# Kernel optimization log

Hardware: AMD Instinct MI355X
Metric: run time of the kernel (lower is better)

## Reference

```python
import jax, jax.numpy as jnp
import numpy as np

EMBED = 1024
HEADS = 16
HEAD_DIM = EMBED // HEADS


def setup_inputs() -> dict:
    key = jax.random.key(0)
    ks = jax.random.split(key, 11)
    B, L, D = 2, 2048, EMBED
    s = 0.02
    return {
        "q": jax.random.normal(ks[0], (B, L, D), jnp.float32),
        "k": jax.random.normal(ks[1], (B, L, D), jnp.float32),
        "v": jax.random.normal(ks[2], (B, L, D), jnp.float32),
        "w_q": jax.random.normal(ks[3], (D, D), jnp.float32) * s,
        "b_q": jnp.zeros((D,), jnp.float32),
        "w_k": jax.random.normal(ks[4], (D, D), jnp.float32) * s,
        "b_k": jnp.zeros((D,), jnp.float32),
        "w_v": jax.random.normal(ks[5], (D, D), jnp.float32) * s,
        "b_v": jnp.zeros((D,), jnp.float32),
        "w_o": jax.random.normal(ks[6], (D, D), jnp.float32) * s,
        "b_o": jnp.zeros((D,), jnp.float32),
    }


def reference(q, k, v, w_q, b_q, w_k, b_k, w_v, b_v, w_o, b_o):
    B, L, D = q.shape
    H, Dh = HEADS, HEAD_DIM
    # Linear projections (torch Linear: x @ W.T + b)
    qp = (q @ w_q.T + b_q).reshape(B, L, H, Dh)
    kp = (k @ w_k.T + b_k).reshape(B, L, H, Dh)
    vp = (v @ w_v.T + b_v).reshape(B, L, H, Dh)
    # energy: [n, h, q, k]
    energy = jnp.einsum("nqhd,nkhd->nhqk", qp, kp)
    scale = 1.0 / jnp.sqrt(jnp.asarray(Dh, qp.dtype))
    attn = jax.nn.softmax(energy * scale, axis=-1)
    ctx = jnp.einsum("nhql,nlhd->nqhd", attn, vp).reshape(B, L, D)
    return ctx @ w_o.T + b_o
```

## Files before the change

kernel.cpp:

```cpp
#include <hip/hip_runtime.h>

typedef __bf16 bf16;
typedef __bf16 bf16x4 __attribute__((ext_vector_type(4)));
typedef __bf16 bf16x8 __attribute__((ext_vector_type(8)));
typedef float f32x4 __attribute__((ext_vector_type(4)));

#define MFMA16(a, b, c) __builtin_amdgcn_mfma_f32_16x16x32_bf16((a), (b), (c), 0, 0, 0)

#define QSCALE 0.18033688011112042f

__device__ inline void gld16(const void* g, void* l) {
    __builtin_amdgcn_global_load_lds(
        (const __attribute__((address_space(1))) unsigned int*)g,
        (__attribute__((address_space(3))) unsigned int*)l, 16, 0, 0);
}

__device__ inline bf16x8 cvt8(float4 a, float4 b) {
    bf16x8 v;
    v[0] = (bf16)a.x; v[1] = (bf16)a.y; v[2] = (bf16)a.z; v[3] = (bf16)a.w;
    v[4] = (bf16)b.x; v[5] = (bf16)b.y; v[6] = (bf16)b.z; v[7] = (bf16)b.w;
    return v;
}

__global__ __launch_bounds__(256) void cvt7_kernel(
    const float* __restrict__ q,  bf16* __restrict__ qb,
    const float* __restrict__ k,  bf16* __restrict__ kb,
    const float* __restrict__ v,  bf16* __restrict__ vb,
    const float* __restrict__ wq, bf16* __restrict__ wqb,
    const float* __restrict__ wk, bf16* __restrict__ wkb,
    const float* __restrict__ wv, bf16* __restrict__ wvb,
    const float* __restrict__ wo, bf16* __restrict__ wob)
{
    const float* src; bf16* dst; int n;
    switch (blockIdx.y) {
        case 0: src = q;  dst = qb;  n = 1 << 22; break;
        case 1: src = k;  dst = kb;  n = 1 << 22; break;
        case 2: src = v;  dst = vb;  n = 1 << 22; break;
        case 3: src = wq; dst = wqb; n = 1 << 20; break;
        case 4: src = wk; dst = wkb; n = 1 << 20; break;
        case 5: src = wv; dst = wvb; n = 1 << 20; break;
        default: src = wo; dst = wob; n = 1 << 20; break;
    }
    int i = (blockIdx.x * 256 + threadIdx.x) * 8;
    if (i < n) {
        float4 a = *(const float4*)&src[i];
        float4 b = *(const float4*)&src[i + 4];
        *(bf16x8*)&dst[i] = cvt8(a, b);
    }
}

__global__ __launch_bounds__(256) void cvt3_kernel(
    const float* __restrict__ s0, bf16* __restrict__ d0,
    const float* __restrict__ s1, bf16* __restrict__ d1,
    const float* __restrict__ s2, bf16* __restrict__ d2)
{
    const float* src = blockIdx.y == 0 ? s0 : blockIdx.y == 1 ? s1 : s2;
    bf16*        dst = blockIdx.y == 0 ? d0 : blockIdx.y == 1 ? d1 : d2;
    int i = (blockIdx.x * 256 + threadIdx.x) * 8;
    float4 a = *(const float4*)&src[i];
    float4 b = *(const float4*)&src[i + 4];
    *(bf16x8*)&dst[i] = cvt8(a, b);
}

__global__ __launch_bounds__(256) void cvt_kernel(
    const float* __restrict__ src, bf16* __restrict__ dst, int n)
{
    int i = (blockIdx.x * 256 + threadIdx.x) * 8;
    if (i < n) {
        float4 a = *(const float4*)&src[i];
        float4 b = *(const float4*)&src[i + 4];
        *(bf16x8*)&dst[i] = cvt8(a, b);
    }
}

__global__ __launch_bounds__(256) void qkv_bf16(
    const bf16* __restrict__ qb, const bf16* __restrict__ kb,
    const bf16* __restrict__ vb,
    const bf16* __restrict__ wq, const float* __restrict__ bq,
    const bf16* __restrict__ wk, const float* __restrict__ bk,
    const bf16* __restrict__ wv, const float* __restrict__ bv,
    bf16* __restrict__ Qp, bf16* __restrict__ Kp, bf16* __restrict__ Vt)
{
    __shared__ __align__(16) bf16 sm[16896];
    bf16* As = sm;
    bf16* Bs = sm + 8192;
    bf16* Ts = sm;

    const int id  = blockIdx.x;
    const int pr  = (id >> 6) * 8 + (id & 7);
    const int proj = pr >> 5;
    const int m0  = (pr & 31) * 128;
    const int n0  = ((id >> 3) & 7) * 128;

    const bf16*  A    = proj == 0 ? qb : proj == 1 ? kb : vb;
    const bf16*  B    = proj == 0 ? wq : proj == 1 ? wk : wv;
    const float* bias = proj == 0 ? bq : proj == 1 ? bk : bv;

    const int tid  = threadIdx.x;
    const int lane = tid & 63;
    const int w    = tid >> 6;
    const int g    = lane >> 4;
    const int ln   = lane & 15;
    const int rowb = (w & 1) * 64;
    const int colb = (w >> 1) * 64;
    const int ro   = lane >> 3, lc = lane & 7;

    auto issue = [&](int t) {
        int k0 = t * 64;
        for (int j = 0; j < 4; ++j) {
            int base = w * 32 + j * 8;
            int row  = base + ro;
            int c    = lc ^ (row & 7);
            gld16(&A[(size_t)(m0 + row) * 1024 + k0 + c * 8], &As[base * 64]);
            gld16(&B[(size_t)(n0 + row) * 1024 + k0 + c * 8], &Bs[base * 64]);
        }
    };

    issue(0);
    f32x4 acc[4][4] = {};

    for (int t = 0; t < 16; ++t) {
        __syncthreads();
        for (int ks = 0; ks < 2; ++ks) {
            bf16x8 af[4], bfm[4];
            for (int mi = 0; mi < 4; ++mi) {
                int row = rowb + mi * 16 + ln;
                af[mi] = *(const bf16x8*)&As[row * 64 + ((ks * 4 + g) ^ (ln & 7)) * 8];
            }
            for (int ni = 0; ni < 4; ++ni) {
                int row = colb + ni * 16 + ln;
                bfm[ni] = *(const bf16x8*)&Bs[row * 64 + ((ks * 4 + g) ^ (ln & 7)) * 8];
            }
            for (int mi = 0; mi < 4; ++mi)
                for (int ni = 0; ni < 4; ++ni)
                    acc[mi][ni] = MFMA16(af[mi], bfm[ni], acc[mi][ni]);
        }
        __syncthreads();
        if (t < 15) issue(t + 1);
    }

    if (proj != 2) {
        for (int mi = 0; mi < 4; ++mi) {
            for (int ni = 0; ni < 4; ++ni) {
                int col = n0 + colb + ni * 16 + ln;
                float bv_ = bias[col];
                int rowbase = m0 + rowb + mi * 16 + g * 4;
                if (proj == 0) {
                    for (int r = 0; r < 4; ++r)
                        Qp[(size_t)(rowbase + r) * 1024 + col] =
                            (bf16)((acc[mi][ni][r] + bv_) * QSCALE);
                } else {
                    for (int r = 0; r < 4; ++r)
                        Kp[(size_t)(rowbase + r) * 1024 + col] =
                            (bf16)(acc[mi][ni][r] + bv_);
                }
            }
        }
    } else {
        for (int mi = 0; mi < 4; ++mi) {
            for (int ni = 0; ni < 4; ++ni) {
                int col = colb + ni * 16 + ln;
                float bv_ = bias[n0 + col];
                int row = rowb + mi * 16 + g * 4;
                bf16x4 pk;
                for (int r = 0; r < 4; ++r) pk[r] = (bf16)(acc[mi][ni][r] + bv_);
                *(bf16x4*)&Ts[col * 132 + row] = pk;
            }
        }
        __syncthreads();
        const int bidx = m0 >> 11;
        const int tok0 = m0 & 2047;
        for (int i = 0; i < 8; ++i) {
            int c    = tid + 256 * i;
            int col  = c >> 4;
            int t64  = (c >> 3) & 1;
            int cc   = c & 7;
            int gcol = n0 + col;
            union { bf16 e[8]; uint4 u; } tmp;
            for (int j = 0; j < 8; ++j) {
                int s = 2 * cc + (j >> 2) + ((j & 3) << 4);
                tmp.e[j] = Ts[col * 132 + t64 * 64 + s];
            }
            size_t dst = ((size_t)(bidx * 16 + (gcol >> 6)) * 64 + (gcol & 63)) * 2048
                         + tok0 + t64 * 64 + cc * 8;
            *(uint4*)&Vt[dst] = tmp.u;
        }
    }
}

__global__ __launch_bounds__(256) void qkv_gemm(
    const float* __restrict__ q, const float* __restrict__ k,
    const float* __restrict__ v,
    const bf16* __restrict__ wq, const float* __restrict__ bq,
    const bf16* __restrict__ wk, const float* __restrict__ bk,
    const bf16* __restrict__ wv, const float* __restrict__ bv,
    bf16* __restrict__ Qp, bf16* __restrict__ Kp, bf16* __restrict__ Vt)
{
    __shared__ __align__(16) bf16 sm[8192 + 2 * 8192];
    bf16* As = sm;
    bf16* Bs = sm + 8192;
    bf16* Ts = sm;

    const int id  = blockIdx.x;
    const int pr  = (id >> 6) * 8 + (id & 7);
    const int proj = pr >> 5;
    const int m0  = (pr & 31) * 128;
    const int n0  = ((id >> 3) & 7) * 128;

    const float* A    = proj == 0 ? q  : proj == 1 ? k  : v;
    const bf16*  B    = proj == 0 ? wq : proj == 1 ? wk : wv;
    const float* bias = proj == 0 ? bq : proj == 1 ? bk : bv;

    const int tid  = threadIdx.x;
    const int lane = tid & 63;
    const int w    = tid >> 6;
    const int g    = lane >> 4;
    const int ln   = lane & 15;
    const int rowb = (w & 1) * 64;
    const int colb = (w >> 1) * 64;
    const int srow = tid >> 3, slc = tid & 7;
    const int ro   = lane >> 3, lc = lane & 7;

    float4 ra[4][2];
    for (int i = 0; i < 4; ++i) {
        const float* p = &A[(size_t)(m0 + srow + 32 * i) * 1024 + slc * 8];
        ra[i][0] = *(const float4*)p;
        ra[i][1] = *(const float4*)(p + 4);
    }
    for (int j = 0; j < 4; ++j) {
        int base = w * 32 + j * 8;
        int row  = base + ro;
        int c    = lc ^ (row & 7);
        gld16(&B[(size_t)(n0 + row) * 1024 + c * 8], &Bs[base * 64]);
    }

    f32x4 acc[4][4] = {};

    for (int t = 0; t < 16; ++t) {
        __syncthreads();
        for (int i = 0; i < 4; ++i) {
            int row = srow + 32 * i;
            *(bf16x8*)&As[row * 64 + (slc ^ (row & 7)) * 8] = cvt8(ra[i][0], ra[i][1]);
        }
        __syncthreads();
        if (t < 15) {
            int k1 = (t + 1) * 64;
            for (int i = 0; i < 4; ++i) {
                const float* p = &A[(size_t)(m0 + srow + 32 * i) * 1024 + k1 + slc * 8];
                ra[i][0] = *(const float4*)p;
                ra[i][1] = *(const float4*)(p + 4);
            }
            int bsel = (t + 1) & 1;
            for (int j = 0; j < 4; ++j) {
                int base = w * 32 + j * 8;
                int row  = base + ro;
                int c    = lc ^ (row & 7);
                gld16(&B[(size_t)(n0 + row) * 1024 + k1 + c * 8],
                      &Bs[bsel * 8192 + base * 64]);
            }
        }
        const bf16* Bt = Bs + (t & 1) * 8192;
        for (int ks = 0; ks < 2; ++ks) {
            bf16x8 af[4], bfm[4];
            for (int mi = 0; mi < 4; ++mi) {
                int row = rowb + mi * 16 + ln;
                af[mi] = *(const bf16x8*)&As[row * 64 + ((ks * 4 + g) ^ (ln & 7)) * 8];
            }
            for (int ni = 0; ni < 4; ++ni) {
                int row = colb + ni * 16 + ln;
                bfm[ni] = *(const bf16x8*)&Bt[row * 64 + ((ks * 4 + g) ^ (ln & 7)) * 8];
            }
            for (int mi = 0; mi < 4; ++mi)
                for (int ni = 0; ni < 4; ++ni)
                    acc[mi][ni] = MFMA16(af[mi], bfm[ni], acc[mi][ni]);
        }
    }

    if (proj != 2) {
        for (int mi = 0; mi < 4; ++mi) {
            for (int ni = 0; ni < 4; ++ni) {
                int col = n0 + colb + ni * 16 + ln;
                float bv_ = bias[col];
                int rowbase = m0 + rowb + mi * 16 + g * 4;
                if (proj == 0) {
                    for (int r = 0; r < 4; ++r)
                        Qp[(size_t)(rowbase + r) * 1024 + col] =
                            (bf16)((acc[mi][ni][r] + bv_) * QSCALE);
                } else {
                    for (int r = 0; r < 4; ++r)
                        Kp[(size_t)(rowbase + r) * 1024 + col] =
                            (bf16)(acc[mi][ni][r] + bv_);
                }
            }
        }
    } else {
        __syncthreads();
        for (int mi = 0; mi < 4; ++mi) {
            for (int ni = 0; ni < 4; ++ni) {
                int col = colb + ni * 16 + ln;
                float bv_ = bias[n0 + col];
                int row = rowb + mi * 16 + g * 4;
                bf16x4 pk;
                for (int r = 0; r < 4; ++r) pk[r] = (bf16)(acc[mi][ni][r] + bv_);
                *(bf16x4*)&Ts[col * 132 + row] = pk;
            }
        }
        __syncthreads();
        const int bidx = m0 >> 11;
        const int tok0 = m0 & 2047;
        for (int i = 0; i < 8; ++i) {
            int c    = tid + 256 * i;
            int col  = c >> 4;
            int t64  = (c >> 3) & 1;
            int cc   = c & 7;
            int gcol = n0 + col;
            union { bf16 e[8]; uint4 u; } tmp;
            for (int j = 0; j < 8; ++j) {
                int s = 2 * cc + (j >> 2) + ((j & 3) << 4);
                tmp.e[j] = Ts[col * 132 + t64 * 64 + s];
            }
            size_t dst = ((size_t)(bidx * 16 + (gcol >> 6)) * 64 + (gcol & 63)) * 2048
                         + tok0 + t64 * 64 + cc * 8;
            *(uint4*)&Vt[dst] = tmp.u;
        }
    }
}

__global__ __launch_bounds__(256) void gemm_out(
    const bf16* __restrict__ A, const bf16* __restrict__ B,
    const float* __restrict__ bias, float* __restrict__ C)
{
    __shared__ __align__(16) bf16 sm[2 * 4096 + 2 * 8192];
    bf16* As = sm;
    bf16* Bs = sm + 8192;

    const int id = blockIdx.x;
    const int m0 = ((id >> 6) * 8 + (id & 7)) * 64;
    const int n0 = ((id >> 3) & 7) * 128;

    const int tid  = threadIdx.x;
    const int lane = tid & 63;
    const int w    = tid >> 6;
    const int g    = lane >> 4;
    const int ln   = lane & 15;
    const int rowb = (w & 1) * 32;
    const int colb = (w >> 1) * 64;
    const int ro   = lane >> 3, lc = lane & 7;

    auto issue = [&](int t) {
        int k0 = t * 64, sel = t & 1;
        for (int j = 0; j < 2; ++j) {
            int base = w * 16 + j * 8;
            int row  = base + ro;
            int c    = lc ^ (row & 7);
            gld16(&A[(size_t)(m0 + row) * 1024 + k0 + c * 8],
                  &As[sel * 4096 + base * 64]);
        }
        for (int j = 0; j < 4; ++j) {
            int base = w * 32 + j * 8;
            int row  = base + ro;
            int c    = lc ^ (row & 7);
            gld16(&B[(size_t)(n0 + row) * 1024 + k0 + c * 8],
                  &Bs[sel * 8192 + base * 64]);
        }
    };

    issue(0);
    f32x4 acc[2][4] = {};

    for (int t = 0; t < 16; ++t) {
        __syncthreads();
        if (t < 15) issue(t + 1);
        const bf16* At = As + (t & 1) * 4096;
        const bf16* Bt = Bs + (t & 1) * 8192;
        for (int ks = 0; ks < 2; ++ks) {
            bf16x8 af[2], bfm[4];
            for (int mi = 0; mi < 2; ++mi) {
                int row = rowb + mi * 16 + ln;
                af[mi] = *(const bf16x8*)&At[row * 64 + ((ks * 4 + g) ^ (ln & 7)) * 8];
            }
            for (int ni = 0; ni < 4; ++ni) {
                int row = colb + ni * 16 + ln;
                bfm[ni] = *(const bf16x8*)&Bt[row * 64 + ((ks * 4 + g) ^ (ln & 7)) * 8];
            }
            for (int mi = 0; mi < 2; ++mi)
                for (int ni = 0; ni < 4; ++ni)
                    acc[mi][ni] = MFMA16(af[mi], bfm[ni], acc[mi][ni]);
        }
    }

    for (int mi = 0; mi < 2; ++mi) {
        for (int ni = 0; ni < 4; ++ni) {
            int col = n0 + colb + ni * 16 + ln;
            float bv_ = bias[col];
            int rowbase = m0 + rowb + mi * 16 + g * 4;
            for (int r = 0; r < 4; ++r)
                C[(size_t)(rowbase + r) * 1024 + col] = acc[mi][ni][r] + bv_;
        }
    }
}

__global__ __launch_bounds__(256) void attn_kernel(
    const bf16* __restrict__ Qp, const bf16* __restrict__ Kp,
    const bf16* __restrict__ Vt, bf16* __restrict__ Ctx)
{
    __shared__ __align__(16) bf16 smem[4096 + 2 * 4096 + 2 * 4096];
    bf16* Ps = smem;
    bf16* Qs = smem;
    bf16* Ks = smem + 4096;
    bf16* Vs = smem + 12288;

    const int id = blockIdx.x;
    const int qt = (id >> 3) & 31;
    const int bh = (id & 7) + ((id >> 8) << 3);

    const int tid  = threadIdx.x;
    const int lane = tid & 63;
    const int w    = tid >> 6;
    const int g    = lane >> 4;
    const int ln   = lane & 15;
    const int ro   = lane >> 3, lc = lane & 7;
    const size_t rowQ0 = (size_t)(bh >> 4) * 2048 + qt * 64;
    const size_t rowK0 = (size_t)(bh >> 4) * 2048;
    const int hcol = (bh & 15) * 64;
    const bf16* VtB = Vt + (size_t)bh * 64 * 2048;

    for (int j = 0; j < 2; ++j) {
        int base = w * 16 + j * 8;
        int row  = base + ro;
        int c    = lc ^ (row & 7);
        gld16(&Qp[(rowQ0 + row) * 1024 + hcol + c * 8], &Qs[base * 64]);
        gld16(&Kp[(rowK0 + row) * 1024 + hcol + c * 8], &Ks[base * 64]);
        gld16(&VtB[(size_t)row * 2048 + c * 8], &Vs[base * 64]);
    }
    __syncthreads();

    bf16x8 qf[2];
    for (int ks = 0; ks < 2; ++ks) {
        int row = w * 16 + ln;
        qf[ks] = *(const bf16x8*)&Qs[row * 64 + ((ks * 4 + g) ^ (ln & 7)) * 8];
    }

    f32x4 oacc[4] = {};
    float l_part[4] = {};

    for (int t = 0; t < 32; ++t) {
        if (t < 31) {
            int sel = (t + 1) & 1, kvo = (t + 1) * 64;
            for (int j = 0; j < 2; ++j) {
                int base = w * 16 + j * 8;
                int kv   = base + ro;
                int c    = lc ^ (kv & 7);
                gld16(&Kp[(rowK0 + kvo + kv) * 1024 + hcol + c * 8],
                      &Ks[sel * 4096 + base * 64]);
                gld16(&VtB[(size_t)kv * 2048 + kvo + c * 8],
                      &Vs[sel * 4096 + base * 64]);
            }
        }
        const bf16* Kt  = Ks + (t & 1) * 4096;
        const bf16* Vti = Vs + (t & 1) * 4096;

        f32x4 sf[4] = {};
        for (int ks = 0; ks < 2; ++ks) {
            bf16x8 kf[4];
            for (int nj = 0; nj < 4; ++nj) {
                int row = nj * 16 + ln;
                kf[nj] = *(const bf16x8*)&Kt[row * 64 + ((ks * 4 + g) ^ (ln & 7)) * 8];
            }
            for (int nj = 0; nj < 4; ++nj)
                sf[nj] = MFMA16(qf[ks], kf[nj], sf[nj]);
        }

        for (int r = 0; r < 4; ++r) {
            float p0 = __builtin_amdgcn_exp2f(sf[0][r]);
            float p1 = __builtin_amdgcn_exp2f(sf[1][r]);
            float p2 = __builtin_amdgcn_exp2f(sf[2][r]);
            float p3 = __builtin_amdgcn_exp2f(sf[3][r]);
            l_part[r] += (p0 + p1) + (p2 + p3);
            int qrow = w * 16 + g * 4 + r;
            int slot = ln ^ ((qrow & 7) << 1);
            bf16x4 pk;
            pk[0] = (bf16)p0; pk[1] = (bf16)p1; pk[2] = (bf16)p2; pk[3] = (bf16)p3;
            *(bf16x4*)&Ps[qrow * 64 + slot * 4] = pk;
        }

        for (int ks = 0; ks < 2; ++ks) {
            bf16x8 pf, vf[4];
            {
                int row = w * 16 + ln;
                int p = (ks * 8 + g * 2) ^ ((row & 7) << 1);
                pf = *(const bf16x8*)&Ps[row * 64 + p * 4];
            }
            for (int nd = 0; nd < 4; ++nd) {
                int row = nd * 16 + ln;
                vf[nd] = *(const bf16x8*)&Vti[row * 64 + ((ks * 4 + g) ^ (ln & 7)) * 8];
            }
            for (int nd = 0; nd < 4; ++nd)
                oacc[nd] = MFMA16(pf, vf[nd], oacc[nd]);
        }
        __syncthreads();
    }

    for (int r = 0; r < 4; ++r) {
        float l = l_part[r];
        for (int off = 8; off >= 1; off >>= 1)
            l += __shfl_xor(l, off, 64);
        float inv = 1.0f / l;
        size_t row = rowQ0 + w * 16 + g * 4 + r;
        for (int nd = 0; nd < 4; ++nd)
            Ctx[row * 1024 + hcol + nd * 16 + ln] = (bf16)(oacc[nd][r] * inv);
    }
}

extern "C" void kernel_launch(void* const* d_in, const int* in_sizes, int n_in,
                              void* d_out, int out_size, void* d_ws, size_t ws_size,
                              hipStream_t stream)
{
    const float* q  = (const float*)d_in[0];
    const float* k  = (const float*)d_in[1];
    const float* v  = (const float*)d_in[2];
    const float* wq = (const float*)d_in[3];
    const float* bq = (const float*)d_in[4];
    const float* wk = (const float*)d_in[5];
    const float* bk = (const float*)d_in[6];
    const float* wv = (const float*)d_in[7];
    const float* bv = (const float*)d_in[8];
    const float* wo = (const float*)d_in[9];
    const float* bo = (const float*)d_in[10];
    float* out = (float*)d_out;

    const int D = 1024;
    bf16* W  = (bf16*)d_ws;
    bf16* Qp = W;
    bf16* Kp = W + (1u << 22);
    bf16* Vt = W + (2u << 22);
    bf16* Ctx = Qp;

    if (ws_size >= (size_t)40 * 1024 * 1024) {
        bf16* vb  = W + (3u << 22);
        bf16* wqb = W + (1u << 24);
        bf16* wkb = wqb + (1u << 20);
        bf16* wvb = wkb + (1u << 20);
        bf16* wob = wvb + (1u << 20);
        bf16* qb  = (bf16*)d_out;
        bf16* kb  = qb + (1u << 22);

        cvt7_kernel<<<dim3(2048, 7), 256, 0, stream>>>(
            q, qb, k, kb, v, vb, wq, wqb, wk, wkb, wv, wvb, wo, wob);
        qkv_bf16<<<768, 256, 0, stream>>>(qb, kb, vb, wqb, bq, wkb, bk, wvb, bv,
                                          Qp, Kp, Vt);
        attn_kernel<<<1024, 256, 0, stream>>>(Qp, Kp, Vt, Ctx);
        gemm_out<<<512, 256, 0, stream>>>(Ctx, wob, bo, out);
    } else {
        bf16* wqb = (bf16*)d_out;
        bf16* wkb = wqb + (size_t)D * D;
        bf16* wvb = wkb + (size_t)D * D;
        bf16* wob = Kp;

        cvt3_kernel<<<dim3(512, 3), 256, 0, stream>>>(wq, wqb, wk, wkb, wv, wvb);
        qkv_gemm<<<768, 256, 0, stream>>>(q, k, v, wqb, bq, wkb, bk, wvb, bv,
                                          Qp, Kp, Vt);
        attn_kernel<<<1024, 256, 0, stream>>>(Qp, Kp, Vt, Ctx);
        cvt_kernel<<<512, 256, 0, stream>>>(wo, wob, D * D);
        gemm_out<<<512, 256, 0, stream>>>(Ctx, wob, bo, out);
    }
}
```

Baseline: 213.9 us.

## Keep attention probabilities in registers via permlane swaps instead of LDS

The score MFMA now computes the transposed S^T (K as A operand), so the exp'd probabilities sit in each lane and can be rearranged into the PV A-operand layout with v_permlane16/32_swap instead of a round trip through shared memory. The row sum is computed by an extra MFMA against a ones vector, removing the shuffle reduction, and Q is loaded straight from global into registers. s_setprio is raised around MFMA bursts. This frees LDS (Ps/Qs region) and removes LDS writes and reads per tile, at the cost of an extra MFMA per k-step and reliance on exact lane-layout correctness.

```diff
diff --git a/kernel.cpp b/kernel.cpp
--- a/kernel.cpp
+++ b/kernel.cpp
@@ -1,6 +1,7 @@
 #include <hip/hip_runtime.h>
 
 typedef __bf16 bf16;
+typedef __bf16 bf16x2 __attribute__((ext_vector_type(2)));
 typedef __bf16 bf16x4 __attribute__((ext_vector_type(4)));
 typedef __bf16 bf16x8 __attribute__((ext_vector_type(8)));
 typedef float f32x4 __attribute__((ext_vector_type(4)));
@@ -404,11 +405,9 @@
     const bf16* __restrict__ Qp, const bf16* __restrict__ Kp,
     const bf16* __restrict__ Vt, bf16* __restrict__ Ctx)
 {
-    __shared__ __align__(16) bf16 smem[4096 + 2 * 4096 + 2 * 4096];
-    bf16* Ps = smem;
-    bf16* Qs = smem;
-    bf16* Ks = smem + 4096;
-    bf16* Vs = smem + 12288;
+    __shared__ __align__(16) bf16 smem[2 * 4096 + 2 * 4096];
+    bf16* Ks = smem;
+    bf16* Vs = smem + 8192;
 
     const int id = blockIdx.x;
     const int qt = (id >> 3) & 31;
@@ -429,20 +428,22 @@
         int base = w * 16 + j * 8;
         int row  = base + ro;
         int c    = lc ^ (row & 7);
-        gld16(&Qp[(rowQ0 + row) * 1024 + hcol + c * 8], &Qs[base * 64]);
         gld16(&Kp[(rowK0 + row) * 1024 + hcol + c * 8], &Ks[base * 64]);
         gld16(&VtB[(size_t)row * 2048 + c * 8], &Vs[base * 64]);
     }
+
+    bf16x8 qf[2];
+    for (int ks = 0; ks < 2; ++ks)
+        qf[ks] = *(const bf16x8*)&Qp[(rowQ0 + w * 16 + ln) * 1024 + hcol
+                                     + ks * 32 + g * 8];
+
+    bf16x8 ones;
+    for (int i = 0; i < 8; ++i) ones[i] = (bf16)1.0f;
+
+    f32x4 oacc[4] = {};
+    f32x4 lacc = {};
+
     __syncthreads();
-
-    bf16x8 qf[2];
-    for (int ks = 0; ks < 2; ++ks) {
-        int row = w * 16 + ln;
-        qf[ks] = *(const bf16x8*)&Qs[row * 64 + ((ks * 4 + g) ^ (ln & 7)) * 8];
-    }
-
-    f32x4 oacc[4] = {};
-    float l_part[4] = {};
 
     for (int t = 0; t < 32; ++t) {
         if (t < 31) {
@@ -467,45 +468,47 @@
                 int row = nj * 16 + ln;
                 kf[nj] = *(const bf16x8*)&Kt[row * 64 + ((ks * 4 + g) ^ (ln & 7)) * 8];
             }
+            __builtin_amdgcn_s_setprio(1);
             for (int nj = 0; nj < 4; ++nj)
-                sf[nj] = MFMA16(qf[ks], kf[nj], sf[nj]);
-        }
-
-        for (int r = 0; r < 4; ++r) {
-            float p0 = __builtin_amdgcn_exp2f(sf[0][r]);
-            float p1 = __builtin_amdgcn_exp2f(sf[1][r]);
-            float p2 = __builtin_amdgcn_exp2f(sf[2][r]);
-            float p3 = __builtin_amdgcn_exp2f(sf[3][r]);
-            l_part[r] += (p0 + p1) + (p2 + p3);
-            int qrow = w * 16 + g * 4 + r;
-            int slot = ln ^ ((qrow & 7) << 1);
-            bf16x4 pk;
-            pk[0] = (bf16)p0; pk[1] = (bf16)p1; pk[2] = (bf16)p2; pk[3] = (bf16)p3;
-            *(bf16x4*)&Ps[qrow * 64 + slot * 4] = pk;
+                sf[nj] = MFMA16(kf[nj], qf[ks], sf[nj]);
+            __builtin_amdgcn_s_setprio(0);
+        }
+
+        unsigned W[4][2];
+        for (int r = 0; r < 4; ++r)
+            for (int h = 0; h < 2; ++h) {
+                bf16x2 t2;
+                t2[0] = (bf16)__builtin_amdgcn_exp2f(sf[2 * h][r]);
+                t2[1] = (bf16)__builtin_amdgcn_exp2f(sf[2 * h + 1][r]);
+                W[r][h] = __builtin_bit_cast(unsigned, t2);
+            }
+        for (int h = 0; h < 2; ++h) {
+            asm("v_permlane16_swap_b32 %0, %1" : "+v"(W[0][h]), "+v"(W[2][h]));
+            asm("v_permlane32_swap_b32 %0, %1" : "+v"(W[0][h]), "+v"(W[2][h]));
+            asm("v_permlane16_swap_b32 %0, %1" : "+v"(W[1][h]), "+v"(W[3][h]));
+            asm("v_permlane32_swap_b32 %0, %1" : "+v"(W[1][h]), "+v"(W[3][h]));
         }
 
         for (int ks = 0; ks < 2; ++ks) {
-            bf16x8 pf, vf[4];
-            {
-                int row = w * 16 + ln;
-                int p = (ks * 8 + g * 2) ^ ((row & 7) << 1);
-                pf = *(const bf16x8*)&Ps[row * 64 + p * 4];
-            }
+            union { unsigned u[4]; bf16x8 v; } pf;
+            pf.u[0] = W[2 * ks][0];     pf.u[1] = W[2 * ks][1];
+            pf.u[2] = W[2 * ks + 1][0]; pf.u[3] = W[2 * ks + 1][1];
+            bf16x8 vf[4];
             for (int nd = 0; nd < 4; ++nd) {
                 int row = nd * 16 + ln;
                 vf[nd] = *(const bf16x8*)&Vti[row * 64 + ((ks * 4 + g) ^ (ln & 7)) * 8];
             }
+            __builtin_amdgcn_s_setprio(1);
+            lacc = MFMA16(pf.v, ones, lacc);
             for (int nd = 0; nd < 4; ++nd)
-                oacc[nd] = MFMA16(pf, vf[nd], oacc[nd]);
+                oacc[nd] = MFMA16(pf.v, vf[nd], oacc[nd]);
+            __builtin_amdgcn_s_setprio(0);
         }
         __syncthreads();
     }
 
     for (int r = 0; r < 4; ++r) {
-        float l = l_part[r];
-        for (int off = 8; off >= 1; off >>= 1)
-            l += __shfl_xor(l, off, 64);
-        float inv = 1.0f / l;
+        float inv = 1.0f / lacc[r];
         size_t row = rowQ0 + w * 16 + g * 4 + r;
         for (int nd = 0; nd < 4; ++nd)
             Ctx[row * 1024 + hcol + nd * 16 + ln] = (bf16)(oacc[nd][r] * inv);
```

New measurement: 221.0 us. +3.3%, slower.
